# Optimization experiments

Hardware: AMD Instinct MI355X
Metric: run time of the kernel (lower is better)

Reference implementation:

```python
import jax, jax.numpy as jnp
import numpy as np

N = 3          # lateral kernel size (odd)
B, R, C, CH = 32, 56, 56, 256  # batch, rows, cols, channels (channels_last)


def setup_inputs() -> dict:
    key = jax.random.key(0)
    k1, k2 = jax.random.split(key)
    x = jax.random.normal(k1, (B, R, C, CH), dtype=jnp.float32)
    kernel = jax.random.normal(k2, (N, N, CH), dtype=jnp.float32) * 0.1
    return {"x": x, "kernel": kernel}


def reference(x, kernel):
    # x: [B, R, C, CH] channels_last; kernel: [n, n, CH] per-channel lateral kernel
    n = kernel.shape[0]
    ch = kernel.shape[2]
    # ZeroCenter constraint: central tap is zero (only lateral connections)
    mask = jnp.ones((n, n, 1), dtype=kernel.dtype).at[n // 2, n // 2, 0].set(0.0)
    k = kernel * mask
    # Depthwise conv, SAME padding == the per-pixel patch batch_dot loop in the original
    k_hwio = k[:, :, None, :]  # [n, n, 1, CH] (I=1 per group)
    out = jax.lax.conv_general_dilated(
        x, k_hwio,
        window_strides=(1, 1),
        padding='SAME',
        dimension_numbers=('NHWC', 'HWIO', 'NHWC'),
        feature_group_count=ch,
    )
    # residual add
    return out + x
```

## Files before the change

### kernel.cpp

```cpp
#include <hip/hip_runtime.h>

#define BB 32
#define RR 56
#define CC 56
#define CHG 64
#define TP 4
#define SEGS (BB * RR * (CC / TP))
#define NBLK (SEGS / 4)

__global__ __launch_bounds__(256) void dwconv3x3_residual2(
    const float4* __restrict__ xv,
    const float4* __restrict__ kv,
    float4* __restrict__ ov)
{
    const int bid = (int)blockIdx.x;
    const int swz = (bid & 7) * (NBLK / 8) + (bid >> 3);
    const int tid = swz * 256 + (int)threadIdx.x;
    const int seg = tid >> 6;
    const int lane = tid & 63;

    const int b   = seg / (RR * (CC / TP));
    const int rem = seg - b * (RR * (CC / TP));
    const int r   = rem / (CC / TP);
    const int cs  = rem - r * (CC / TP);
    const int c0  = cs * TP;

    float4 kt[9];
    #pragma unroll
    for (int t = 0; t < 9; ++t)
        kt[t] = kv[t * CHG + lane];

    float4 row[3][TP + 2];
    const int pixbase = (b * RR + r) * CC + c0;

    const bool interior = (r > 0) & (r < RR - 1) & (cs > 0) & (cs < (CC / TP) - 1);
    if (interior) {
        #pragma unroll
        for (int dr = 0; dr < 3; ++dr) {
            const int rowbase = (pixbase + (dr - 1) * CC - 1) * CHG + lane;
            #pragma unroll
            for (int j = 0; j < TP + 2; ++j)
                row[dr][j] = xv[rowbase + j * CHG];
        }
    } else {
        #pragma unroll
        for (int dr = 0; dr < 3; ++dr) {
            const int rr2 = r + dr - 1;
            #pragma unroll
            for (int j = 0; j < TP + 2; ++j) {
                const int cc2 = c0 + j - 1;
                float4 v = make_float4(0.f, 0.f, 0.f, 0.f);
                if (rr2 >= 0 && rr2 < RR && cc2 >= 0 && cc2 < CC)
                    v = xv[((b * RR + rr2) * CC + cc2) * CHG + lane];
                row[dr][j] = v;
            }
        }
    }

    #pragma unroll
    for (int p = 0; p < TP; ++p) {
        float4 acc = row[1][p + 1];
        #pragma unroll
        for (int dr = 0; dr < 3; ++dr) {
            #pragma unroll
            for (int dc = 0; dc < 3; ++dc) {
                if (dr == 1 && dc == 1) continue;
                const float4 kk = kt[dr * 3 + dc];
                const float4 xx = row[dr][p + dc];
                acc.x += kk.x * xx.x;
                acc.y += kk.y * xx.y;
                acc.z += kk.z * xx.z;
                acc.w += kk.w * xx.w;
            }
        }
        ov[(pixbase + p) * CHG + lane] = acc;
    }
}

extern "C" void kernel_launch(void* const* d_in, const int* in_sizes, int n_in,
                              void* d_out, int out_size, void* d_ws, size_t ws_size,
                              hipStream_t stream)
{
    const float4* xv = (const float4*)d_in[0];
    const float4* kv = (const float4*)d_in[1];
    float4* ov       = (float4*)d_out;

    dwconv3x3_residual2<<<NBLK, 256, 0, stream>>>(xv, kv, ov);
}
```

Baseline: 35.73 us.

## Tile 4x4 pixels per thread with rolling row buffers for vertical reuse

Each thread now computes a 4x4 spatial tile instead of a 1x4 strip. It streams input rows through a four-row rotating register buffer, so each input row is loaded once and reused across three output rows. This cuts redundant global and L2 loads from 18 to 6 per output row, and the grid shrinks by four. The cost is more registers per thread and fewer blocks, which could lower occupancy or latency hiding on a kernel that is mostly memory-bound.

```diff
diff --git a/kernel.cpp b/kernel.cpp
--- a/kernel.cpp
+++ b/kernel.cpp
@@ -4,11 +4,65 @@
 #define RR 56
 #define CC 56
 #define CHG 64
-#define TP 4
-#define SEGS (BB * RR * (CC / TP))
+#define TPC 4
+#define TPR 4
+#define CSEG (CC / TPC)
+#define RSEG (RR / TPR)
+#define SEGS (BB * RSEG * CSEG)
 #define NBLK (SEGS / 4)
 
-__global__ __launch_bounds__(256) void dwconv3x3_residual2(
+__device__ __forceinline__ void load_row(float4 dst[6], const float4* __restrict__ xv, int base) {
+    #pragma unroll
+    for (int j = 0; j < 6; ++j) dst[j] = xv[base + j * CHG];
+}
+
+__device__ __forceinline__ void load_row_guarded(float4 dst[6], const float4* __restrict__ xv,
+                                                 int b, int r, int c0, int lane) {
+    const bool rok = (r >= 0) & (r < RR);
+    const int base = ((b * RR + r) * CC + c0 - 1) * CHG + lane;
+    #pragma unroll
+    for (int j = 0; j < 6; ++j) {
+        const int cc = c0 - 1 + j;
+        float4 v = make_float4(0.f, 0.f, 0.f, 0.f);
+        if (rok && cc >= 0 && cc < CC) v = xv[base + j * CHG];
+        dst[j] = v;
+    }
+}
+
+__device__ __forceinline__ void compute_store(float4* __restrict__ ov, int obase,
+                                              const float4 kt[9],
+                                              const float4 up[6], const float4 mid[6],
+                                              const float4 dn[6]) {
+    #pragma unroll
+    for (int p = 0; p < TPC; ++p) {
+        float4 acc = mid[p + 1];
+        #pragma unroll
+        for (int dc = 0; dc < 3; ++dc) {
+            const float4 ku = kt[dc];
+            const float4 xu = up[p + dc];
+            acc.x += ku.x * xu.x; acc.y += ku.y * xu.y;
+            acc.z += ku.z * xu.z; acc.w += ku.w * xu.w;
+        }
+        {
+            const float4 k0 = kt[3], k2 = kt[5];
+            const float4 x0 = mid[p], x2 = mid[p + 2];
+            acc.x += k0.x * x0.x + k2.x * x2.x;
+            acc.y += k0.y * x0.y + k2.y * x2.y;
+            acc.z += k0.z * x0.z + k2.z * x2.z;
+            acc.w += k0.w * x0.w + k2.w * x2.w;
+        }
+        #pragma unroll
+        for (int dc = 0; dc < 3; ++dc) {
+            const float4 kd = kt[6 + dc];
+            const float4 xd = dn[p + dc];
+            acc.x += kd.x * xd.x; acc.y += kd.y * xd.y;
+            acc.z += kd.z * xd.z; acc.w += kd.w * xd.w;
+        }
+        ov[obase + p * CHG] = acc;
+    }
+}
+
+__global__ __launch_bounds__(256) void dwconv3x3_res3(
     const float4* __restrict__ xv,
     const float4* __restrict__ kv,
     float4* __restrict__ ov)
@@ -19,61 +73,49 @@
     const int seg = tid >> 6;
     const int lane = tid & 63;
 
-    const int b   = seg / (RR * (CC / TP));
-    const int rem = seg - b * (RR * (CC / TP));
-    const int r   = rem / (CC / TP);
-    const int cs  = rem - r * (CC / TP);
-    const int c0  = cs * TP;
+    const int b   = seg / (RSEG * CSEG);
+    const int rem = seg - b * (RSEG * CSEG);
+    const int rs  = rem / CSEG;
+    const int cs  = rem - rs * CSEG;
+    const int r0  = rs * TPR;
+    const int c0  = cs * TPC;
 
     float4 kt[9];
     #pragma unroll
     for (int t = 0; t < 9; ++t)
-        kt[t] = kv[t * CHG + lane];
+        if (t != 4) kt[t] = kv[t * CHG + lane];
 
-    float4 row[3][TP + 2];
-    const int pixbase = (b * RR + r) * CC + c0;
+    const int ibase = (b * RR + r0) * CC + c0;
+    const int rowstride = CC * CHG;
+    const int obase = ibase * CHG + lane;
 
-    const bool interior = (r > 0) & (r < RR - 1) & (cs > 0) & (cs < (CC / TP) - 1);
+    float4 buf0[6], buf1[6], buf2[6], buf3[6];
+
+    const bool interior = (rs > 0) & (rs < RSEG - 1) & (cs > 0) & (cs < CSEG - 1);
+
     if (interior) {
-        #pragma unroll
-        for (int dr = 0; dr < 3; ++dr) {
-            const int rowbase = (pixbase + (dr - 1) * CC - 1) * CHG + lane;
-            #pragma unroll
-            for (int j = 0; j < TP + 2; ++j)
-                row[dr][j] = xv[rowbase + j * CHG];
-        }
+        const int bm1 = (ibase - CC - 1) * CHG + lane;
+        load_row(buf0, xv, bm1);
+        load_row(buf1, xv, bm1 + rowstride);
+        load_row(buf2, xv, bm1 + 2 * rowstride);
+        load_row(buf3, xv, bm1 + 3 * rowstride);
+        compute_store(ov, obase,                kt, buf0, buf1, buf2);
+        load_row(buf0, xv, bm1 + 4 * rowstride);
+        compute_store(ov, obase + rowstride,    kt, buf1, buf2, buf3);
+        load_row(buf1, xv, bm1 + 5 * rowstride);
+        compute_store(ov, obase + 2 * rowstride, kt, buf2, buf3, buf0);
+        compute_store(ov, obase + 3 * rowstride, kt, buf3, buf0, buf1);
     } else {
-        #pragma unroll
-        for (int dr = 0; dr < 3; ++dr) {
-            const int rr2 = r + dr - 1;
-            #pragma unroll
-            for (int j = 0; j < TP + 2; ++j) {
-                const int cc2 = c0 + j - 1;
-                float4 v = make_float4(0.f, 0.f, 0.f, 0.f);
-                if (rr2 >= 0 && rr2 < RR && cc2 >= 0 && cc2 < CC)
-                    v = xv[((b * RR + rr2) * CC + cc2) * CHG + lane];
-                row[dr][j] = v;
-            }
-        }
-    }
-
-    #pragma unroll
-    for (int p = 0; p < TP; ++p) {
-        float4 acc = row[1][p + 1];
-        #pragma unroll
-        for (int dr = 0; dr < 3; ++dr) {
-            #pragma unroll
-            for (int dc = 0; dc < 3; ++dc) {
-                if (dr == 1 && dc == 1) continue;
-                const float4 kk = kt[dr * 3 + dc];
-                const float4 xx = row[dr][p + dc];
-                acc.x += kk.x * xx.x;
-                acc.y += kk.y * xx.y;
-                acc.z += kk.z * xx.z;
-                acc.w += kk.w * xx.w;
-            }
-        }
-        ov[(pixbase + p) * CHG + lane] = acc;
+        load_row_guarded(buf0, xv, b, r0 - 1, c0, lane);
+        load_row_guarded(buf1, xv, b, r0,     c0, lane);
+        load_row_guarded(buf2, xv, b, r0 + 1, c0, lane);
+        load_row_guarded(buf3, xv, b, r0 + 2, c0, lane);
+        compute_store(ov, obase,                kt, buf0, buf1, buf2);
+        load_row_guarded(buf0, xv, b, r0 + 3, c0, lane);
+        compute_store(ov, obase + rowstride,    kt, buf1, buf2, buf3);
+        load_row_guarded(buf1, xv, b, r0 + 4, c0, lane);
+        compute_store(ov, obase + 2 * rowstride, kt, buf2, buf3, buf0);
+        compute_store(ov, obase + 3 * rowstride, kt, buf3, buf0, buf1);
     }
 }
 
@@ -85,5 +127,5 @@
     const float4* kv = (const float4*)d_in[1];
     float4* ov       = (float4*)d_out;
 
-    dwconv3x3_residual2<<<NBLK, 256, 0, stream>>>(xv, kv, ov);
+    dwconv3x3_res3<<<NBLK, 256, 0, stream>>>(xv, kv, ov);
 }
```

Result: slower. 37.40 us (+4.7%).
